# Kernel optimization log

Measured on AMD Instinct MI355X. Metric: run time of the kernel, lower is better.

Reference implementation:

```python
import jax, jax.numpy as jnp
import numpy as np

B, N, S, D_IN, D_OUT = 8, 8192, 8, 64, 64


def setup_inputs() -> dict:
    key = jax.random.key(0)
    ks = jax.random.split(key, 7)
    x = jax.random.normal(ks[0], (B, N, D_IN), dtype=jnp.float32)
    j_idx = jax.random.randint(ks[1], (B, N, S), 0, N, dtype=jnp.int32)
    k_idx = jax.random.randint(ks[2], (B, N, S), 0, N, dtype=jnp.int32)
    # MLP params: Linear(3d -> 2d), GELU, Linear(2d -> d_out)
    s1 = 1.0 / np.sqrt(3 * D_IN)
    s2 = 1.0 / np.sqrt(2 * D_IN)
    W1 = jax.random.uniform(ks[3], (3 * D_IN, 2 * D_IN), jnp.float32, -s1, s1)
    b1 = jax.random.uniform(ks[4], (2 * D_IN,), jnp.float32, -s1, s1)
    W2 = jax.random.uniform(ks[5], (2 * D_IN, D_OUT), jnp.float32, -s2, s2)
    b2 = jax.random.uniform(ks[6], (D_OUT,), jnp.float32, -s2, s2)
    return {"x": x, "j_idx": j_idx, "k_idx": k_idx, "W1": W1, "b1": b1, "W2": W2, "b2": b2}


def reference(x, j_idx, k_idx, W1, b1, W2, b2):
    # x: (B,N,D); j_idx/k_idx: (B,N,S) indices into N
    gather = jax.vmap(lambda xb, ib: xb[ib])  # per-batch gather -> (N,S,D)
    xj = gather(x, j_idx)                      # (B,N,S,D)
    xk = gather(x, k_idx)                      # (B,N,S,D)
    xi = jnp.broadcast_to(x[:, :, None, :], xj.shape)
    triple = jnp.concatenate([xi, xj, xk], axis=-1)  # (B,N,S,3D)
    h = jax.nn.gelu(triple @ W1 + b1, approximate=False)  # (B,N,S,2D)
    out = h @ W2 + b2                                       # (B,N,S,D_OUT)
    return out.mean(axis=2)                                 # (B,N,D_OUT)
```

## Files before the change

kernel.cpp:

```cpp
#include <hip/hip_runtime.h>
#include <stdint.h>


#define NT   4
#define NBLK 2048

typedef short  short8 __attribute__((ext_vector_type(8)));
typedef float  f32x4  __attribute__((ext_vector_type(4)));
typedef float  f32x16 __attribute__((ext_vector_type(16)));

__device__ __forceinline__ unsigned short f2bf(float f){
  union { float f; unsigned u; } a; a.f = f;
  unsigned u = a.u;
  u += 0x7fffu + ((u >> 16) & 1u);
  return (unsigned short)(u >> 16);
}
__device__ __forceinline__ float fast_gelu(float x){
  float x2 = x * x;
  float t  = __builtin_fmaf(x2, -0.1029437f, -2.3022083f);
  float p  = __builtin_amdgcn_exp2f(x * t);
  return x * __builtin_amdgcn_rcpf(1.0f + p);
}

__global__ void prep_kernel(const float* __restrict__ x, const float* __restrict__ W1,
                            const float* __restrict__ W2, short* __restrict__ xb,
                            short* __restrict__ w1f, short* __restrict__ w2f){
  int bid = blockIdx.x;
  if (bid < 2048){
    long i = (long)bid * 256 + threadIdx.x;
    const float4* p = (const float4*)(x + i * 8);
    float4 a = p[0], b = p[1];
    short8 v;
    v[0]=(short)f2bf(a.x); v[1]=(short)f2bf(a.y); v[2]=(short)f2bf(a.z); v[3]=(short)f2bf(a.w);
    v[4]=(short)f2bf(b.x); v[5]=(short)f2bf(b.y); v[6]=(short)f2bf(b.z); v[7]=(short)f2bf(b.w);
    *(short8*)(xb + i * 8) = v;
  } else if (threadIdx.x < 64){
    int f = bid - 2048, lane = threadIdx.x;
    short8 v;
    if (f < 48){
      int cb = f / 12, t = f % 12;
      #pragma unroll
      for (int j = 0; j < 8; j++)
        v[j] = (short)f2bf(W1[(t*16 + 8*(lane>>5) + j)*128 + cb*32 + (lane&31)]);
      *(short8*)(w1f + ((long)(f*64 + lane))*8) = v;
    } else {
      int g = f - 48; int w = g >> 2, q = g & 3;
      #pragma unroll
      for (int j = 0; j < 8; j++)
        v[j] = (short)f2bf(W2[(q*32 + 8*(lane>>4) + j)*64 + w*16 + (lane&15)]);
      *(short8*)(w2f + ((long)(g*64 + lane))*8) = v;
    }
  }
}

__device__ __forceinline__ void stage_tile(short* buf, const short* xb, long tb,
                                           int jn, int kn, int w, int lane){
  long token = tb + lane;
  int own = (int)(token >> 3);
  int bb  = (int)((token >> 16) << 13);
  int jr = bb + jn, kr = bb + kn;
  #pragma unroll
  for (int v = 0; v < 3; v++){
    int kg = w + 8 * v;
    int src = (v == 0) ? own : ((v == 1) ? jr : kr);
    const short* gp = xb + (long)src * 64 + w * 8;
    __builtin_amdgcn_global_load_lds(
        (const __attribute__((address_space(1))) unsigned int*)gp,
        (__attribute__((address_space(3))) unsigned int*)(buf + kg * 512),
        16, 0, 0);
  }
}

__global__ __launch_bounds__(512, 4) void ltc_main(
    const short* __restrict__ xb,  const short* __restrict__ w1f,
    const short* __restrict__ w2f, const int* __restrict__ jidx,
    const int* __restrict__ kidx,  const float* __restrict__ b1,
    const float* __restrict__ b2,  float* __restrict__ out)
{
  __shared__ short Ab[2][24 * 512];
  __shared__ short HB[16 * 136];

  const int tid  = threadIdx.x;
  const int w    = tid >> 6, lane = tid & 63;
  const int cb   = w & 3,  rb  = w >> 2;
  const int l31  = lane & 31, hi = lane >> 5;
  const int l15  = lane & 15, q4 = lane >> 4;

  short8 w1v[12];
  #pragma unroll
  for (int t = 0; t < 12; t++)
    w1v[t] = *(const short8*)(w1f + ((long)((cb * 12 + t) * 64 + lane)) * 8);
  short8 w2v[4];
  #pragma unroll
  for (int q = 0; q < 4; q++)
    w2v[q] = *(const short8*)(w2f + ((long)(((w & 3) * 4 + q) * 64 + lane)) * 8);

  float b1v = b1[cb * 32 + l31];
  float b2v = b2[(w & 3) * 16 + l15];

  for (int i = tid; i < 8 * 136; i += 512) HB[8 * 136 + i] = 0;

  int bid  = blockIdx.x;
  int T0   = (bid & 7) * 1024 + (bid >> 3) * NT;
  long tb0 = (long)T0 * 64;

  int jn = jidx[tb0 + lane], kn = kidx[tb0 + lane];
  stage_tile(&Ab[0][0], xb, tb0, jn, kn, w, lane);
  int jn1 = 0, kn1 = 0;
  if (NT > 1){ jn1 = jidx[tb0 + 64 + lane]; kn1 = kidx[tb0 + 64 + lane]; }

  int cur = 0;
  for (int tt = 0; tt < NT; ++tt){
    asm volatile("s_waitcnt vmcnt(0)\n\ts_barrier" ::: "memory");
    if (tt + 1 < NT)
      stage_tile(&Ab[cur ^ 1][0], xb, tb0 + (long)(tt + 1) * 64, jn1, kn1, w, lane);
    if (tt + 2 < NT){
      jn1 = jidx[tb0 + (long)(tt + 2) * 64 + lane];
      kn1 = kidx[tb0 + (long)(tt + 2) * 64 + lane];
    }

    const short* Ac = &Ab[cur][0];
    f32x16 acc;
    #pragma unroll
    for (int r = 0; r < 16; r++) acc[r] = b1v;
    #pragma unroll
    for (int t = 0; t < 12; t++){
      short8 afr = *(const short8*)(Ac + ((2 * t + hi) * 64 + rb * 32 + l31) * 8);
      acc = __builtin_amdgcn_mfma_f32_32x32x16_bf16(afr, w1v[t], acc, 0, 0, 0);
    }

    float hbv[4];
    #pragma unroll
    for (int o = 0; o < 4; o++){
      float s0 = fast_gelu(acc[4*o+0]);
      s0 += fast_gelu(acc[4*o+1]);
      s0 += fast_gelu(acc[4*o+2]);
      s0 += fast_gelu(acc[4*o+3]);
      float other = __shfl_xor(s0, 32);
      hbv[o] = (s0 + other) * 0.125f;
    }
    if (hi == 0){
      #pragma unroll
      for (int o = 0; o < 4; o++)
        HB[(rb * 4 + o) * 136 + cb * 32 + l31] = (short)f2bf(hbv[o]);
    }
    asm volatile("s_waitcnt lgkmcnt(0)\n\ts_barrier" ::: "memory");

    if (w < 4){
      f32x4 acc2 = {0.f, 0.f, 0.f, 0.f};
      #pragma unroll
      for (int q = 0; q < 4; q++){
        short8 hbf = *(const short8*)(HB + l15 * 136 + q * 32 + q4 * 8);
        acc2 = __builtin_amdgcn_mfma_f32_16x16x32_bf16(hbf, w2v[q], acc2, 0, 0, 0);
      }
      if (lane < 32){
        long G = ((long)(T0 + tt)) * 8;
        #pragma unroll
        for (int r = 0; r < 4; r++)
          out[(G + 4 * q4 + r) * 64 + (w & 3) * 16 + l15] = acc2[r] + b2v;
      }
    }
    cur ^= 1;
  }
}

__global__ void ltc_naive(const float* __restrict__ x, const int* __restrict__ jidx,
                          const int* __restrict__ kidx, const float* __restrict__ W1,
                          const float* __restrict__ b1, const float* __restrict__ W2,
                          const float* __restrict__ b2, float* __restrict__ out)
{
  int gidx = blockIdx.x;
  int b = gidx >> 13;
  __shared__ float trip[8][192];
  __shared__ float hb[128];
  int t = threadIdx.x;
  for (int i = t; i < 8 * 192; i += 128){
    int s = i / 192, c = i - s * 192;
    int v = c >> 6, cc = c & 63;
    int src;
    if (v == 0)      src = gidx & 8191;
    else if (v == 1) src = jidx[gidx * 8 + s];
    else             src = kidx[gidx * 8 + s];
    trip[s][c] = x[((long)(b << 13) + src) * 64 + cc];
  }
  __syncthreads();
  float z[8];
  #pragma unroll
  for (int s = 0; s < 8; s++) z[s] = b1[t];
  for (int k = 0; k < 192; k++){
    float w = W1[k * 128 + t];
    #pragma unroll
    for (int s = 0; s < 8; s++) z[s] = fmaf(trip[s][k], w, z[s]);
  }
  float acc = 0.f;
  #pragma unroll
  for (int s = 0; s < 8; s++) acc += fast_gelu(z[s]);
  hb[t] = acc * 0.125f;
  __syncthreads();
  if (t < 64){
    float o = b2[t];
    for (int h = 0; h < 128; h++) o = fmaf(hb[h], W2[h * 64 + t], o);
    out[(long)gidx * 64 + t] = o;
  }
}

extern "C" void kernel_launch(void* const* d_in, const int* in_sizes, int n_in,
                              void* d_out, int out_size, void* d_ws, size_t ws_size,
                              hipStream_t stream) {
  const float* x   = (const float*)d_in[0];
  const int*   jix = (const int*)  d_in[1];
  const int*   kix = (const int*)  d_in[2];
  const float* W1  = (const float*)d_in[3];
  const float* b1  = (const float*)d_in[4];
  const float* W2  = (const float*)d_in[5];
  const float* b2  = (const float*)d_in[6];
  float* out = (float*)d_out;

  const size_t xb_elems  = (size_t)8 * 8192 * 64;
  const size_t w1f_elems = 48 * 64 * 8;
  const size_t w2f_elems = 16 * 64 * 8;
  const size_t need = (xb_elems + w1f_elems + w2f_elems) * sizeof(short);

  if (ws_size >= need){
    short* xb  = (short*)d_ws;
    short* w1f = xb + xb_elems;
    short* w2f = w1f + w1f_elems;
    prep_kernel<<<2112, 256, 0, stream>>>(x, W1, W2, xb, w1f, w2f);
    ltc_main<<<NBLK, 512, 0, stream>>>(xb, w1f, w2f, jix, kix, b1, b2, out);
  } else {
    ltc_naive<<<8 * 8192, 128, 0, stream>>>(x, jix, kix, W1, b1, W2, b2, out);
  }
}
```

Before: 60.08 us.

## Load gathered A fragments directly into registers, drop LDS staging and double-buffer HB

```diff
diff --git a/kernel.cpp b/kernel.cpp
--- a/kernel.cpp
+++ b/kernel.cpp
@@ -2,8 +2,8 @@
 #include <stdint.h>
 
 
-#define NT   4
-#define NBLK 2048
+#define NT   8
+#define NBLK 1024
 
 typedef short  short8 __attribute__((ext_vector_type(8)));
 typedef float  f32x4  __attribute__((ext_vector_type(4)));
@@ -53,32 +53,14 @@
   }
 }
 
-__device__ __forceinline__ void stage_tile(short* buf, const short* xb, long tb,
-                                           int jn, int kn, int w, int lane){
-  long token = tb + lane;
-  int own = (int)(token >> 3);
-  int bb  = (int)((token >> 16) << 13);
-  int jr = bb + jn, kr = bb + kn;
-  #pragma unroll
-  for (int v = 0; v < 3; v++){
-    int kg = w + 8 * v;
-    int src = (v == 0) ? own : ((v == 1) ? jr : kr);
-    const short* gp = xb + (long)src * 64 + w * 8;
-    __builtin_amdgcn_global_load_lds(
-        (const __attribute__((address_space(1))) unsigned int*)gp,
-        (__attribute__((address_space(3))) unsigned int*)(buf + kg * 512),
-        16, 0, 0);
-  }
-}
-
 __global__ __launch_bounds__(512, 4) void ltc_main(
     const short* __restrict__ xb,  const short* __restrict__ w1f,
     const short* __restrict__ w2f, const int* __restrict__ jidx,
     const int* __restrict__ kidx,  const float* __restrict__ b1,
     const float* __restrict__ b2,  float* __restrict__ out)
 {
-  __shared__ short Ab[2][24 * 512];
-  __shared__ short HB[16 * 136];
+  __shared__ short HB[2][16 * 136];
+  __shared__ short W2S[16 * 64 * 8];
 
   const int tid  = threadIdx.x;
   const int w    = tid >> 6, lane = tid & 63;
@@ -90,44 +72,49 @@
   #pragma unroll
   for (int t = 0; t < 12; t++)
     w1v[t] = *(const short8*)(w1f + ((long)((cb * 12 + t) * 64 + lane)) * 8);
-  short8 w2v[4];
-  #pragma unroll
-  for (int q = 0; q < 4; q++)
-    w2v[q] = *(const short8*)(w2f + ((long)(((w & 3) * 4 + q) * 64 + lane)) * 8);
+
+  for (int i = tid; i < 16 * 64; i += 512)
+    *(short8*)&W2S[i * 8] = *(const short8*)(w2f + (long)i * 8);
 
   float b1v = b1[cb * 32 + l31];
-  float b2v = b2[(w & 3) * 16 + l15];
-
-  for (int i = tid; i < 8 * 136; i += 512) HB[8 * 136 + i] = 0;
+  float b2v = b2[cb * 16 + l15];
+
+  for (int i = tid; i < 8 * 136; i += 512){ HB[0][8*136 + i] = 0; HB[1][8*136 + i] = 0; }
 
   int bid  = blockIdx.x;
   int T0   = (bid & 7) * 1024 + (bid >> 3) * NT;
   long tb0 = (long)T0 * 64;
 
-  int jn = jidx[tb0 + lane], kn = kidx[tb0 + lane];
-  stage_tile(&Ab[0][0], xb, tb0, jn, kn, w, lane);
-  int jn1 = 0, kn1 = 0;
-  if (NT > 1){ jn1 = jidx[tb0 + 64 + lane]; kn1 = kidx[tb0 + 64 + lane]; }
-
-  int cur = 0;
+  const int tokOff = rb * 32 + l31;
+  int jnC = jidx[tb0 + tokOff], knC = kidx[tb0 + tokOff];
+
   for (int tt = 0; tt < NT; ++tt){
-    asm volatile("s_waitcnt vmcnt(0)\n\ts_barrier" ::: "memory");
-    if (tt + 1 < NT)
-      stage_tile(&Ab[cur ^ 1][0], xb, tb0 + (long)(tt + 1) * 64, jn1, kn1, w, lane);
-    if (tt + 2 < NT){
-      jn1 = jidx[tb0 + (long)(tt + 2) * 64 + lane];
-      kn1 = kidx[tb0 + (long)(tt + 2) * 64 + lane];
-    }
-
-    const short* Ac = &Ab[cur][0];
+    long tb  = tb0 + (long)tt * 64;
+    int tok  = (int)tb + tokOff;
+    int own  = tok >> 3;
+    int bb   = (tok >> 16) << 13;
+    const short* baseO = xb + (long)own * 64 + 8 * hi;
+    const short* baseJ = xb + (long)(bb + jnC) * 64 + 8 * hi;
+    const short* baseK = xb + (long)(bb + knC) * 64 + 8 * hi;
+
+    short8 af[12];
+    #pragma unroll
+    for (int t2 = 0; t2 < 4; t2++){
+      af[t2]     = *(const short8*)(baseO + 16 * t2);
+      af[4 + t2] = *(const short8*)(baseJ + 16 * t2);
+      af[8 + t2] = *(const short8*)(baseK + 16 * t2);
+    }
+    if (tt + 1 < NT){
+      jnC = jidx[tb + 64 + tokOff];
+      knC = kidx[tb + 64 + tokOff];
+    }
+
     f32x16 acc;
     #pragma unroll
     for (int r = 0; r < 16; r++) acc[r] = b1v;
     #pragma unroll
-    for (int t = 0; t < 12; t++){
-      short8 afr = *(const short8*)(Ac + ((2 * t + hi) * 64 + rb * 32 + l31) * 8);
-      acc = __builtin_amdgcn_mfma_f32_32x32x16_bf16(afr, w1v[t], acc, 0, 0, 0);
-    }
+    for (int t = 0; t < 12; t++)
+      acc = __builtin_amdgcn_mfma_f32_32x32x16_bf16(af[t], w1v[t], acc, 0, 0, 0);
 
     float hbv[4];
     #pragma unroll
@@ -142,7 +129,7 @@
     if (hi == 0){
       #pragma unroll
       for (int o = 0; o < 4; o++)
-        HB[(rb * 4 + o) * 136 + cb * 32 + l31] = (short)f2bf(hbv[o]);
+        HB[tt & 1][(rb * 4 + o) * 136 + cb * 32 + l31] = (short)f2bf(hbv[o]);
     }
     asm volatile("s_waitcnt lgkmcnt(0)\n\ts_barrier" ::: "memory");
 
@@ -150,17 +137,17 @@
       f32x4 acc2 = {0.f, 0.f, 0.f, 0.f};
       #pragma unroll
       for (int q = 0; q < 4; q++){
-        short8 hbf = *(const short8*)(HB + l15 * 136 + q * 32 + q4 * 8);
-        acc2 = __builtin_amdgcn_mfma_f32_16x16x32_bf16(hbf, w2v[q], acc2, 0, 0, 0);
+        short8 hbf = *(const short8*)&HB[tt & 1][l15 * 136 + q * 32 + q4 * 8];
+        short8 w2r = *(const short8*)&W2S[((w * 4 + q) * 64 + lane) * 8];
+        acc2 = __builtin_amdgcn_mfma_f32_16x16x32_bf16(hbf, w2r, acc2, 0, 0, 0);
       }
       if (lane < 32){
         long G = ((long)(T0 + tt)) * 8;
         #pragma unroll
         for (int r = 0; r < 4; r++)
-          out[(G + 4 * q4 + r) * 64 + (w & 3) * 16 + l15] = acc2[r] + b2v;
+          out[(G + 4 * q4 + r) * 64 + w * 16 + l15] = acc2[r] + b2v;
       }
     }
-    cur ^= 1;
   }
 }
 
@@ -188,9 +175,9 @@
   #pragma unroll
   for (int s = 0; s < 8; s++) z[s] = b1[t];
   for (int k = 0; k < 192; k++){
-    float w = W1[k * 128 + t];
-    #pragma unroll
-    for (int s = 0; s < 8; s++) z[s] = fmaf(trip[s][k], w, z[s]);
+    float wv = W1[k * 128 + t];
+    #pragma unroll
+    for (int s = 0; s < 8; s++) z[s] = fmaf(trip[s][k], wv, z[s]);
   }
   float acc = 0.f;
   #pragma unroll
```

Result: slower. 87.48 us (+45.6%).
